# Kernel optimization log

Measured on AMD Instinct MI355X. Metric: run time of the kernel, lower is better.

## Reference

```python
import jax, jax.numpy as jnp
import numpy as np

B, C, H, W = 64, 512, 32, 32


def _conv1x1(x, w):
    # x: [B,C,H,W], w: [Cout,Cin] (1x1 conv kernel squeezed) -> [B,Cout,H,W]
    return jnp.einsum('bchw,oc->bohw', x, w)


def _spike(v, threshold):
    # Single-timestep LIF with fresh state: mem = decay*0 + v = v; fire where mem >= threshold.
    # Binary spike output (membrane reset after fire is irrelevant for one step).
    return (v >= threshold).astype(v.dtype)


def setup_inputs() -> dict:
    key = jax.random.key(0)
    ks = jax.random.split(key, 5)
    xavier = 1.0 / np.sqrt(C)  # xavier_normal std for square 1x1 conv: sqrt(2/(C+C))
    return {
        'x': jax.random.normal(ks[0], (B, C, H, W), dtype=jnp.float32),
        'w_sieve1': jax.random.normal(ks[1], (C, C), dtype=jnp.float32) * xavier,
        'w_sieve2': jax.random.normal(ks[2], (C, C), dtype=jnp.float32) * xavier,
        'w_source': jax.random.normal(ks[3], (C, C), dtype=jnp.float32) * xavier,
        'w_lin': jax.random.normal(ks[4], (C, C), dtype=jnp.float32) * xavier,
    }


def reference(x, w_sieve1, w_sieve2, w_source, w_lin):
    # lif_input called with threshold override = 1
    x_in = _spike(x, 1.0)                               # binary spikes [B,C,H,W]
    x_res = x_in
    source = _spike(_conv1x1(x_in, w_source), 1.0)      # lif_source, threshold=1.0 (min=0 clamp inert: 1.0>0)
    sieve = _spike(_conv1x1(x_in, w_sieve1) + _conv1x1(x_in, w_sieve2), 4.0)  # lif_Sieve, threshold=4.0
    gated = sieve * source                              # spike-gated activation
    out = (_conv1x1(gated, w_lin) + x_res) * 0.5
    return out
```

## Files before the change

kernel.cpp:

```cpp
#include <hip/hip_runtime.h>
#include <hip/hip_bf16.h>

#define WL_CAP 65536u

typedef __attribute__((ext_vector_type(4))) int i32x4;
typedef __attribute__((ext_vector_type(4))) float f32x4v;
typedef __attribute__((ext_vector_type(4))) unsigned short u16x4v;

__global__ void prep_wsum_i8(const float* __restrict__ w1, const float* __restrict__ w2,
                             char* __restrict__ wsum) {
  int i = (blockIdx.x * 256 + threadIdx.x) * 4;
  float4 a = *reinterpret_cast<const float4*>(w1 + i);
  float4 b = *reinterpret_cast<const float4*>(w2 + i);
  int v0 = __float2int_rn(fminf(fmaxf((a.x + b.x) * 256.f, -127.f), 127.f));
  int v1 = __float2int_rn(fminf(fmaxf((a.y + b.y) * 256.f, -127.f), 127.f));
  int v2 = __float2int_rn(fminf(fmaxf((a.z + b.z) * 256.f, -127.f), 127.f));
  int v3 = __float2int_rn(fminf(fmaxf((a.w + b.w) * 256.f, -127.f), 127.f));
  unsigned u = (v0 & 0xFF) | ((v1 & 0xFF) << 8) | ((v2 & 0xFF) << 16) | ((v3 & 0xFF) << 24);
  *reinterpret_cast<unsigned*>(wsum + i) = u;
}

__global__ __launch_bounds__(256) void spike_pack_direct(const float* __restrict__ x,
                                                         float* __restrict__ out,
                                                         unsigned short* __restrict__ xinb16) {
  int t = threadIdx.x;
  int g = blockIdx.x;
  int b = g >> 5, cg = g & 31;
  int px = t * 4;
  size_t rowbase = ((size_t)(b * 512 + cg * 16)) * 1024 + (size_t)px;

  f32x4v v[16];
#pragma unroll
  for (int ci = 0; ci < 16; ++ci)
    v[ci] = *reinterpret_cast<const f32x4v*>(x + rowbase + (size_t)ci * 1024);

  unsigned u0 = 0, u1 = 0, u2 = 0, u3 = 0;
#pragma unroll
  for (int ci = 0; ci < 16; ++ci) {
    unsigned s0 = (v[ci].x >= 1.f) ? 1u : 0u;
    unsigned s1 = (v[ci].y >= 1.f) ? 1u : 0u;
    unsigned s2 = (v[ci].z >= 1.f) ? 1u : 0u;
    unsigned s3 = (v[ci].w >= 1.f) ? 1u : 0u;
    f32x4v ov;
    ov.x = 0.5f * (float)s0; ov.y = 0.5f * (float)s1;
    ov.z = 0.5f * (float)s2; ov.w = 0.5f * (float)s3;
    __builtin_nontemporal_store(ov, reinterpret_cast<f32x4v*>(out + rowbase + (size_t)ci * 1024));
    u0 |= s0 << ci; u1 |= s1 << ci; u2 |= s2 << ci; u3 |= s3 << ci;
  }
  u16x4v o;
  o.x = (unsigned short)u0; o.y = (unsigned short)u1;
  o.z = (unsigned short)u2; o.w = (unsigned short)u3;
  __builtin_nontemporal_store(o, reinterpret_cast<u16x4v*>(
      xinb16 + (size_t)cg * 65536 + (size_t)(b * 1024 + px)));
}

__global__ __launch_bounds__(256) void gemm_fire_i8(const char* __restrict__ wsum,
                                                    const unsigned short* __restrict__ xinb16,
                                                    unsigned* __restrict__ counter,
                                                    unsigned* __restrict__ wl) {
  __shared__ char As[128 * 512];
  int m0 = blockIdx.x * 128;
  int n0 = blockIdx.y * 128;
  int t = threadIdx.x;
  int lane = t & 63;
  int wv = t >> 6;
  int wr = wv >> 1, wc = wv & 1;
  int fr = lane & 15;
  int kgrp = lane >> 4;

#pragma unroll
  for (int i = 0; i < 16; ++i) {
    int idx = t + i * 256;
    int row = idx >> 5;
    int col16 = (idx & 31) * 16;
    int scol = col16 ^ ((row & 7) << 4);
    const char* ga = wsum + (size_t)(m0 + row) * 512 + scol;
    __builtin_amdgcn_global_load_lds((const __attribute__((address_space(1))) void*)ga,
                                     (__attribute__((address_space(3))) void*)(As + idx * 16),
                                     16, 0, 0);
  }

  unsigned short bbits[4][8];
#pragma unroll
  for (int ni = 0; ni < 4; ++ni) {
    int prow = n0 + wc * 64 + ni * 16 + fr;
#pragma unroll
    for (int kt = 0; kt < 8; ++kt)
      bbits[ni][kt] = xinb16[(size_t)(kt * 4 + kgrp) * 65536 + prow];
  }

  i32x4 acc[4][4];
#pragma unroll
  for (int i = 0; i < 4; ++i)
#pragma unroll
    for (int j = 0; j < 4; ++j) acc[i][j] = (i32x4){0, 0, 0, 0};

  __syncthreads();

#pragma unroll
  for (int kt = 0; kt < 8; ++kt) {
    i32x4 av[4];
#pragma unroll
    for (int mi = 0; mi < 4; ++mi) {
      int row = wr * 64 + mi * 16 + fr;
      int col = (kt * 64 + kgrp * 16) ^ ((row & 7) << 4);
      av[mi] = *reinterpret_cast<const i32x4*>(&As[row * 512 + col]);
    }
#pragma unroll
    for (int ni = 0; ni < 4; ++ni) {
      unsigned s = bbits[ni][kt];
      i32x4 bv;
      bv[0] = (int)((((s      ) & 0xFu) * 0x00204081u) & 0x01010101u);
      bv[1] = (int)((((s >>  4) & 0xFu) * 0x00204081u) & 0x01010101u);
      bv[2] = (int)((((s >>  8) & 0xFu) * 0x00204081u) & 0x01010101u);
      bv[3] = (int)((((s >> 12) & 0xFu) * 0x00204081u) & 0x01010101u);
#pragma unroll
      for (int mi = 0; mi < 4; ++mi)
        acc[mi][ni] = __builtin_amdgcn_mfma_i32_16x16x64_i8(av[mi], bv, acc[mi][ni], 0, 0, 0);
    }
  }

  int rowg = (lane >> 4) * 4;
#pragma unroll
  for (int mi = 0; mi < 4; ++mi)
#pragma unroll
    for (int ni = 0; ni < 4; ++ni)
#pragma unroll
      for (int v = 0; v < 4; ++v) {
        if (acc[mi][ni][v] >= 896) {
          unsigned o = (unsigned)(m0 + wr * 64 + mi * 16 + rowg + v);
          unsigned p = (unsigned)(n0 + wc * 64 + ni * 16 + fr);
          unsigned slot = atomicAdd(counter, 1u);
          if (slot < WL_CAP) wl[slot] = (o << 16) | p;
        }
      }
}

__global__ void finish_fires(const float* __restrict__ x, const float* __restrict__ w1,
                             const float* __restrict__ w2, const float* __restrict__ wsrc,
                             const float* __restrict__ wlin, float* __restrict__ out,
                             const unsigned* __restrict__ counter,
                             const unsigned* __restrict__ wl) {
  unsigned n = *counter;
  if (n > WL_CAP) n = WL_CAP;
  for (unsigned i = blockIdx.x * blockDim.x + threadIdx.x; i < n;
       i += gridDim.x * blockDim.x) {
    unsigned e = wl[i];
    int o = (int)(e >> 16);
    int p = (int)(e & 0xFFFFu);
    int b = p >> 10, hw = p & 1023;
    const float* xb = x + (size_t)b * 512 * 1024 + hw;
    float s1 = 0.f, s2 = 0.f;
    for (int c = 0; c < 512; ++c) {
      if (xb[(size_t)c * 1024] >= 1.f) {
        s1 += w1[o * 512 + c] + w2[o * 512 + c];
        s2 += wsrc[o * 512 + c];
      }
    }
    if (s1 >= 4.0f && s2 >= 1.0f) {
      for (int c = 0; c < 512; ++c)
        atomicAdd(&out[((size_t)b * 512 + c) * 1024 + hw], 0.5f * wlin[c * 512 + o]);
    }
  }
}

__global__ void fallback_dense(const float* __restrict__ x, const float* __restrict__ w1,
                               const float* __restrict__ w2, const float* __restrict__ wsrc,
                               const float* __restrict__ wlin, float* __restrict__ out) {
  __shared__ float xin[512];
  __shared__ float gated[512];
  int p = blockIdx.x;
  int b = p >> 10, hw = p & 1023;
  const float* xb = x + (size_t)b * 512 * 1024 + hw;
  for (int c = threadIdx.x; c < 512; c += 256)
    xin[c] = (xb[(size_t)c * 1024] >= 1.f) ? 1.f : 0.f;
  __syncthreads();
  for (int o = threadIdx.x; o < 512; o += 256) {
    float s1 = 0.f, s2 = 0.f;
    for (int c = 0; c < 512; ++c) {
      float xv = xin[c];
      s1 += xv * (w1[o * 512 + c] + w2[o * 512 + c]);
      s2 += xv * wsrc[o * 512 + c];
    }
    gated[o] = (s1 >= 4.f && s2 >= 1.f) ? 1.f : 0.f;
  }
  __syncthreads();
  for (int c = threadIdx.x; c < 512; c += 256) {
    float a = 0.f;
    for (int o = 0; o < 512; ++o) a += gated[o] * wlin[c * 512 + o];
    out[((size_t)b * 512 + c) * 1024 + hw] = 0.5f * (a + xin[c]);
  }
}

extern "C" void kernel_launch(void* const* d_in, const int* in_sizes, int n_in,
                              void* d_out, int out_size, void* d_ws, size_t ws_size,
                              hipStream_t stream) {
  const float* x    = (const float*)d_in[0];
  const float* w1   = (const float*)d_in[1];
  const float* w2   = (const float*)d_in[2];
  const float* wsrc = (const float*)d_in[3];
  const float* wlin = (const float*)d_in[4];
  float* out = (float*)d_out;

  const size_t NEED = (size_t)8 * 1024 * 1024;
  if (ws_size >= NEED) {
    unsigned* counter = (unsigned*)d_ws;
    unsigned* wl = (unsigned*)((char*)d_ws + 1024);
    char* wsum_i8 = (char*)d_ws + (1u << 20);
    unsigned short* xinb16 = (unsigned short*)((char*)d_ws + (2u << 20));

    (void)hipMemsetAsync(d_ws, 0, 4, stream);
    prep_wsum_i8<<<256, 256, 0, stream>>>(w1, w2, wsum_i8);
    spike_pack_direct<<<2048, 256, 0, stream>>>(x, out, xinb16);
    gemm_fire_i8<<<dim3(4, 512), 256, 0, stream>>>(wsum_i8, xinb16, counter, wl);
    finish_fires<<<dim3(32), 64, 0, stream>>>(x, w1, w2, wsrc, wlin, out, counter, wl);
  } else {
    fallback_dense<<<65536, 256, 0, stream>>>(x, w1, w2, wsrc, wlin, out);
  }
}
```

Before: 77.02 us.

## Split residual output write from spike packing into separate expand kernel

The spike packing kernel no longer writes the 0.5*spike residual to the output. It now only reads x and emits the 16-bit packed spike masks with a normal store. A new expand_out kernel, launched after the GEMM, rebuilds the residual output from the packed bits with nontemporal stores. The likely aim is to make the packing pass read-only so the GEMM can start sooner and the output write is decoupled, at the cost of an extra launch and a re-read of the small packed buffer.

```diff
diff --git a/kernel.cpp b/kernel.cpp
--- a/kernel.cpp
+++ b/kernel.cpp
@@ -20,9 +20,8 @@
   *reinterpret_cast<unsigned*>(wsum + i) = u;
 }
 
-__global__ __launch_bounds__(256) void spike_pack_direct(const float* __restrict__ x,
-                                                         float* __restrict__ out,
-                                                         unsigned short* __restrict__ xinb16) {
+__global__ __launch_bounds__(256) void spike_pack_ro(const float* __restrict__ x,
+                                                     unsigned short* __restrict__ xinb16) {
   int t = threadIdx.x;
   int g = blockIdx.x;
   int b = g >> 5, cg = g & 31;
@@ -37,21 +36,37 @@
   unsigned u0 = 0, u1 = 0, u2 = 0, u3 = 0;
 #pragma unroll
   for (int ci = 0; ci < 16; ++ci) {
-    unsigned s0 = (v[ci].x >= 1.f) ? 1u : 0u;
-    unsigned s1 = (v[ci].y >= 1.f) ? 1u : 0u;
-    unsigned s2 = (v[ci].z >= 1.f) ? 1u : 0u;
-    unsigned s3 = (v[ci].w >= 1.f) ? 1u : 0u;
-    f32x4v ov;
-    ov.x = 0.5f * (float)s0; ov.y = 0.5f * (float)s1;
-    ov.z = 0.5f * (float)s2; ov.w = 0.5f * (float)s3;
-    __builtin_nontemporal_store(ov, reinterpret_cast<f32x4v*>(out + rowbase + (size_t)ci * 1024));
-    u0 |= s0 << ci; u1 |= s1 << ci; u2 |= s2 << ci; u3 |= s3 << ci;
+    u0 |= ((v[ci].x >= 1.f) ? 1u : 0u) << ci;
+    u1 |= ((v[ci].y >= 1.f) ? 1u : 0u) << ci;
+    u2 |= ((v[ci].z >= 1.f) ? 1u : 0u) << ci;
+    u3 |= ((v[ci].w >= 1.f) ? 1u : 0u) << ci;
   }
   u16x4v o;
   o.x = (unsigned short)u0; o.y = (unsigned short)u1;
   o.z = (unsigned short)u2; o.w = (unsigned short)u3;
-  __builtin_nontemporal_store(o, reinterpret_cast<u16x4v*>(
-      xinb16 + (size_t)cg * 65536 + (size_t)(b * 1024 + px)));
+  *reinterpret_cast<u16x4v*>(xinb16 + (size_t)cg * 65536 + (size_t)(b * 1024 + px)) = o;
+}
+
+__global__ __launch_bounds__(256) void expand_out(const unsigned short* __restrict__ xinb16,
+                                                  float* __restrict__ out) {
+  int tid = blockIdx.x * 256 + threadIdx.x;
+#pragma unroll
+  for (int it = 0; it < 16; ++it) {
+    int i = tid + it * 524288;
+    int e4 = i << 2;
+    int px = e4 & 1023;
+    int c  = (e4 >> 10) & 511;
+    int b  = e4 >> 19;
+    u16x4v m = *reinterpret_cast<const u16x4v*>(
+        xinb16 + (size_t)(c >> 4) * 65536 + (size_t)(b << 10) + px);
+    int bit = c & 15;
+    f32x4v ov;
+    ov.x = ((m.x >> bit) & 1) ? 0.5f : 0.0f;
+    ov.y = ((m.y >> bit) & 1) ? 0.5f : 0.0f;
+    ov.z = ((m.z >> bit) & 1) ? 0.5f : 0.0f;
+    ov.w = ((m.w >> bit) & 1) ? 0.5f : 0.0f;
+    __builtin_nontemporal_store(ov, reinterpret_cast<f32x4v*>(out + e4));
+  }
 }
 
 __global__ __launch_bounds__(256) void gemm_fire_i8(const char* __restrict__ wsum,
@@ -211,8 +226,9 @@
 
     (void)hipMemsetAsync(d_ws, 0, 4, stream);
     prep_wsum_i8<<<256, 256, 0, stream>>>(w1, w2, wsum_i8);
-    spike_pack_direct<<<2048, 256, 0, stream>>>(x, out, xinb16);
+    spike_pack_ro<<<2048, 256, 0, stream>>>(x, xinb16);
     gemm_fire_i8<<<dim3(4, 512), 256, 0, stream>>>(wsum_i8, xinb16, counter, wl);
+    expand_out<<<2048, 256, 0, stream>>>(xinb16, out);
     finish_fires<<<dim3(32), 64, 0, stream>>>(x, w1, w2, wsrc, wlin, out, counter, wl);
   } else {
     fallback_dense<<<65536, 256, 0, stream>>>(x, w1, w2, wsrc, wlin, out);
```

Result: slower. 84.27 us (+9.4%).

## Pack input spikes with wave ballots and transpose bits in GEMM via LDS

Applied to the files above, without the earlier changes.

The spike packing kernel now reads one channel row per wave with coalesced scalar loads and uses ballot to produce 64-pixel bit words per channel, instead of 16-channel-per-pixel shorts built from float4 loads. The GEMM loads these bit words into LDS with async global-to-LDS copies and transposes them in registers into per-pixel 16-channel masks for the int8 MFMA B operand. The aim is smaller, better-coalesced bitmask traffic and fewer scattered 2-byte global loads in the GEMM. In exchange the GEMM does extra per-k-tile bit-extraction ALU work, and the output stores are no longer nontemporal or vectorised.

```diff
diff --git a/kernel.cpp b/kernel.cpp
--- a/kernel.cpp
+++ b/kernel.cpp
@@ -4,8 +4,6 @@
 #define WL_CAP 65536u
 
 typedef __attribute__((ext_vector_type(4))) int i32x4;
-typedef __attribute__((ext_vector_type(4))) float f32x4v;
-typedef __attribute__((ext_vector_type(4))) unsigned short u16x4v;
 
 __global__ void prep_wsum_i8(const float* __restrict__ w1, const float* __restrict__ w2,
                              char* __restrict__ wsum) {
@@ -20,47 +18,46 @@
   *reinterpret_cast<unsigned*>(wsum + i) = u;
 }
 
-__global__ __launch_bounds__(256) void spike_pack_direct(const float* __restrict__ x,
-                                                         float* __restrict__ out,
-                                                         unsigned short* __restrict__ xinb16) {
+__global__ __launch_bounds__(256) void spike_ballot(const float* __restrict__ x,
+                                                    float* __restrict__ out,
+                                                    unsigned long long* __restrict__ bw) {
   int t = threadIdx.x;
-  int g = blockIdx.x;
-  int b = g >> 5, cg = g & 31;
-  int px = t * 4;
-  size_t rowbase = ((size_t)(b * 512 + cg * 16)) * 1024 + (size_t)px;
-
-  f32x4v v[16];
-#pragma unroll
-  for (int ci = 0; ci < 16; ++ci)
-    v[ci] = *reinterpret_cast<const f32x4v*>(x + rowbase + (size_t)ci * 1024);
-
-  unsigned u0 = 0, u1 = 0, u2 = 0, u3 = 0;
-#pragma unroll
-  for (int ci = 0; ci < 16; ++ci) {
-    unsigned s0 = (v[ci].x >= 1.f) ? 1u : 0u;
-    unsigned s1 = (v[ci].y >= 1.f) ? 1u : 0u;
-    unsigned s2 = (v[ci].z >= 1.f) ? 1u : 0u;
-    unsigned s3 = (v[ci].w >= 1.f) ? 1u : 0u;
-    f32x4v ov;
-    ov.x = 0.5f * (float)s0; ov.y = 0.5f * (float)s1;
-    ov.z = 0.5f * (float)s2; ov.w = 0.5f * (float)s3;
-    __builtin_nontemporal_store(ov, reinterpret_cast<f32x4v*>(out + rowbase + (size_t)ci * 1024));
-    u0 |= s0 << ci; u1 |= s1 << ci; u2 |= s2 << ci; u3 |= s3 << ci;
-  }
-  u16x4v o;
-  o.x = (unsigned short)u0; o.y = (unsigned short)u1;
-  o.z = (unsigned short)u2; o.w = (unsigned short)u3;
-  __builtin_nontemporal_store(o, reinterpret_cast<u16x4v*>(
-      xinb16 + (size_t)cg * 65536 + (size_t)(b * 1024 + px)));
+  int lane = t & 63, wave = t >> 6;
+  int rowblk = blockIdx.x * 16;
+#pragma unroll
+  for (int iter = 0; iter < 16; ++iter) {
+    int task = wave + iter * 4;
+    int row = rowblk + (task >> 2);
+    int q = task & 3;
+    size_t base = (size_t)row * 1024 + q * 256 + lane;
+    float v0 = x[base];
+    float v1 = x[base + 64];
+    float v2 = x[base + 128];
+    float v3 = x[base + 192];
+    unsigned long long b0 = __ballot(v0 >= 1.f);
+    unsigned long long b1 = __ballot(v1 >= 1.f);
+    unsigned long long b2 = __ballot(v2 >= 1.f);
+    unsigned long long b3 = __ballot(v3 >= 1.f);
+    out[base]       = (v0 >= 1.f) ? 0.5f : 0.f;
+    out[base + 64]  = (v1 >= 1.f) ? 0.5f : 0.f;
+    out[base + 128] = (v2 >= 1.f) ? 0.5f : 0.f;
+    out[base + 192] = (v3 >= 1.f) ? 0.5f : 0.f;
+    if (lane < 4) {
+      unsigned long long my = (lane == 0) ? b0 : (lane == 1) ? b1 : (lane == 2) ? b2 : b3;
+      bw[(size_t)row * 16 + q * 4 + lane] = my;
+    }
+  }
 }
 
 __global__ __launch_bounds__(256) void gemm_fire_i8(const char* __restrict__ wsum,
-                                                    const unsigned short* __restrict__ xinb16,
+                                                    const unsigned long long* __restrict__ bw,
                                                     unsigned* __restrict__ counter,
                                                     unsigned* __restrict__ wl) {
   __shared__ char As[128 * 512];
+  __shared__ unsigned long long Bw[512][2];
   int m0 = blockIdx.x * 128;
   int n0 = blockIdx.y * 128;
+  int b = n0 >> 10, hw0 = n0 & 1023;
   int t = threadIdx.x;
   int lane = t & 63;
   int wv = t >> 6;
@@ -79,14 +76,13 @@
                                      (__attribute__((address_space(3))) void*)(As + idx * 16),
                                      16, 0, 0);
   }
-
-  unsigned short bbits[4][8];
-#pragma unroll
-  for (int ni = 0; ni < 4; ++ni) {
-    int prow = n0 + wc * 64 + ni * 16 + fr;
-#pragma unroll
-    for (int kt = 0; kt < 8; ++kt)
-      bbits[ni][kt] = xinb16[(size_t)(kt * 4 + kgrp) * 65536 + prow];
+#pragma unroll
+  for (int i = 0; i < 2; ++i) {
+    int idx = t + i * 256;
+    const char* gb = (const char*)(bw + (size_t)(b * 512 + idx) * 16 + (hw0 >> 6));
+    __builtin_amdgcn_global_load_lds((const __attribute__((address_space(1))) void*)gb,
+                                     (__attribute__((address_space(3))) void*)((char*)Bw + idx * 16),
+                                     16, 0, 0);
   }
 
   i32x4 acc[4][4];
@@ -106,14 +102,24 @@
       int col = (kt * 64 + kgrp * 16) ^ ((row & 7) << 4);
       av[mi] = *reinterpret_cast<const i32x4*>(&As[row * 512 + col]);
     }
+    unsigned s[4] = {0u, 0u, 0u, 0u};
+    int cbase = kt * 64 + kgrp * 16;
+#pragma unroll
+    for (int ci = 0; ci < 16; ++ci) {
+      unsigned long long w = Bw[cbase + ci][wc];
+      s[0] |= (unsigned)((w >> (fr)) & 1ull) << ci;
+      s[1] |= (unsigned)((w >> (16 + fr)) & 1ull) << ci;
+      s[2] |= (unsigned)((w >> (32 + fr)) & 1ull) << ci;
+      s[3] |= (unsigned)((w >> (48 + fr)) & 1ull) << ci;
+    }
 #pragma unroll
     for (int ni = 0; ni < 4; ++ni) {
-      unsigned s = bbits[ni][kt];
+      unsigned sv = s[ni];
       i32x4 bv;
-      bv[0] = (int)((((s      ) & 0xFu) * 0x00204081u) & 0x01010101u);
-      bv[1] = (int)((((s >>  4) & 0xFu) * 0x00204081u) & 0x01010101u);
-      bv[2] = (int)((((s >>  8) & 0xFu) * 0x00204081u) & 0x01010101u);
-      bv[3] = (int)((((s >> 12) & 0xFu) * 0x00204081u) & 0x01010101u);
+      bv[0] = (int)((((sv      ) & 0xFu) * 0x00204081u) & 0x01010101u);
+      bv[1] = (int)((((sv >>  4) & 0xFu) * 0x00204081u) & 0x01010101u);
+      bv[2] = (int)((((sv >>  8) & 0xFu) * 0x00204081u) & 0x01010101u);
+      bv[3] = (int)((((sv >> 12) & 0xFu) * 0x00204081u) & 0x01010101u);
 #pragma unroll
       for (int mi = 0; mi < 4; ++mi)
         acc[mi][ni] = __builtin_amdgcn_mfma_i32_16x16x64_i8(av[mi], bv, acc[mi][ni], 0, 0, 0);
@@ -207,12 +213,12 @@
     unsigned* counter = (unsigned*)d_ws;
     unsigned* wl = (unsigned*)((char*)d_ws + 1024);
     char* wsum_i8 = (char*)d_ws + (1u << 20);
-    unsigned short* xinb16 = (unsigned short*)((char*)d_ws + (2u << 20));
+    unsigned long long* bwp = (unsigned long long*)((char*)d_ws + (2u << 20));
 
     (void)hipMemsetAsync(d_ws, 0, 4, stream);
     prep_wsum_i8<<<256, 256, 0, stream>>>(w1, w2, wsum_i8);
-    spike_pack_direct<<<2048, 256, 0, stream>>>(x, out, xinb16);
-    gemm_fire_i8<<<dim3(4, 512), 256, 0, stream>>>(wsum_i8, xinb16, counter, wl);
+    spike_ballot<<<2048, 256, 0, stream>>>(x, out, bwp);
+    gemm_fire_i8<<<dim3(4, 512), 256, 0, stream>>>(wsum_i8, bwp, counter, wl);
     finish_fires<<<dim3(32), 64, 0, stream>>>(x, w1, w2, wsrc, wlin, out, counter, wl);
   } else {
     fallback_dense<<<65536, 256, 0, stream>>>(x, w1, w2, wsrc, wlin, out);
```

Result: slower. 110.8 us (+43.8%).
